# Kernel optimization log

Measured on AMD Instinct MI355X. Metric: run time of the kernel, lower is better.

Reference implementation:

```python
import jax, jax.numpy as jnp
import numpy as np

N_NODES = 150000
N_EDGES = 2400000
N_GRAPHS = 1024
EPS = 1e-5


def setup_inputs() -> dict:
    key = jax.random.key(0)
    ks = jax.random.split(key, 20)
    x = jax.random.normal(ks[0], (N_NODES, 3), dtype=jnp.float32)
    edge_index = jax.random.randint(ks[1], (2, N_EDGES), 0, N_NODES, dtype=jnp.int64)
    batch = jnp.sort(jax.random.randint(ks[2], (N_NODES,), 0, N_GRAPHS, dtype=jnp.int64))

    def glorot(k, shape):
        fan_in, fan_out = shape[0], shape[1]
        lim = jnp.sqrt(6.0 / (fan_in + fan_out)).astype(jnp.float32)
        return jax.random.uniform(k, shape, jnp.float32, -lim, lim)

    params = dict(
        W1=glorot(ks[3], (3, 32)), b1=jnp.zeros((32,), jnp.float32),
        gn1_w=jnp.ones((32,), jnp.float32), gn1_b=jnp.zeros((32,), jnp.float32), gn1_ms=jnp.ones((32,), jnp.float32),
        W2=glorot(ks[4], (32, 32)), b2=jnp.zeros((32,), jnp.float32),
        gn2_w=jnp.ones((32,), jnp.float32), gn2_b=jnp.zeros((32,), jnp.float32), gn2_ms=jnp.ones((32,), jnp.float32),
        W3=glorot(ks[5], (32, 32)), b3=jnp.zeros((32,), jnp.float32),
        gn3_w=jnp.ones((32,), jnp.float32), gn3_b=jnp.zeros((32,), jnp.float32), gn3_ms=jnp.ones((32,), jnp.float32),
        lin_w=glorot(ks[6], (32, 3)), lin_b=jnp.zeros((3,), jnp.float32),
    )
    return dict(x=x, edge_index=edge_index, batch=batch, **params)


def _gcn_conv(x, W, b, src, dst, dinv_sqrt):
    # PyG GCNConv: h = x @ W; propagate with sym-normalized A + self-loops; + bias
    h = x @ W  # [N, F]
    coef = dinv_sqrt[src] * dinv_sqrt[dst]  # [E]
    msgs = h[src] * coef[:, None]  # [E, F]
    agg = jax.ops.segment_sum(msgs, dst, num_segments=N_NODES)
    agg = agg + (dinv_sqrt * dinv_sqrt)[:, None] * h  # self-loop term
    return agg + b


def _graph_norm(x, batch, counts, weight, bias, mean_scale):
    # PyG GraphNorm: per-graph mean/var with learnable mean_scale
    mean = jax.ops.segment_sum(x, batch, num_segments=N_GRAPHS) / counts[:, None]
    out = x - mean_scale * mean[batch]
    var = jax.ops.segment_sum(out * out, batch, num_segments=N_GRAPHS) / counts[:, None]
    std = jnp.sqrt(var + EPS)
    return weight * out / std[batch] + bias


def reference(x, edge_index, batch,
              W1, b1, gn1_w, gn1_b, gn1_ms,
              W2, b2, gn2_w, gn2_b, gn2_ms,
              W3, b3, gn3_w, gn3_b, gn3_ms,
              lin_w, lin_b):
    src, dst = edge_index[0], edge_index[1]
    # degree over A + I (edge weight 1)
    deg = jax.ops.segment_sum(jnp.ones((N_EDGES,), jnp.float32), dst, num_segments=N_NODES) + 1.0
    dinv_sqrt = jax.lax.rsqrt(deg)
    counts = jax.ops.segment_sum(jnp.ones((N_NODES,), jnp.float32), batch, num_segments=N_GRAPHS)

    x1 = jax.nn.relu(_graph_norm(_gcn_conv(x, W1, b1, src, dst, dinv_sqrt), batch, counts, gn1_w, gn1_b, gn1_ms))
    h2 = _graph_norm(_gcn_conv(x1, W2, b2, src, dst, dinv_sqrt), batch, counts, gn2_w, gn2_b, gn2_ms)
    x2 = jax.nn.relu(h2 + x1)
    h3 = _graph_norm(_gcn_conv(x2, W3, b3, src, dst, dinv_sqrt), batch, counts, gn3_w, gn3_b, gn3_ms)
    x3 = jax.nn.relu(h3 + x2)

    pooled = jax.ops.segment_sum(x3, batch, num_segments=N_GRAPHS) / counts[:, None]  # mean pool
    return pooled @ lin_w + lin_b  # [G, 3]
```

## Files before the change

kernel.cpp:

```cpp
#include <hip/hip_runtime.h>

#define N_NODES 150000
#define N_EDGES 2400000
#define N_GRAPHS 1024
#define F 32
#define EPSV 1e-5f

#define BS 256
#define NB ((N_NODES + BS - 1) / BS)
#define CAP 5120
#define EB 8192
#define NEB ((N_EDGES + EB - 1) / EB)
#define EPT (EB / 256)
#define KPT (CAP / 256)

#define SSH 14
#define NS 10

__device__ __forceinline__ float bflo(unsigned int u) {
    union { unsigned int i; float f; } v; v.i = u << 16; return v.f;
}
__device__ __forceinline__ float bfhi(unsigned int u) {
    union { unsigned int i; float f; } v; v.i = u & 0xffff0000u; return v.f;
}
__device__ __forceinline__ unsigned int f2bf(float f) {
    union { float f; unsigned int i; } v; v.f = f;
    unsigned int r = v.i + 0x7fff + ((v.i >> 16) & 1);
    return r >> 16;
}

__global__ void k_init(const int* __restrict__ batch, int* __restrict__ bucketCur,
                       int* __restrict__ off, float* __restrict__ gstats) {
    int i = blockIdx.x * blockDim.x + threadIdx.x;
    if (i >= N_NODES) return;
    if (i < NB) bucketCur[i] = i * CAP;
    if (i < N_GRAPHS * 9) gstats[i] = 0.f;
    int b = batch[i];
    if (i == 0) {
        for (int g = 0; g <= b; ++g) off[g] = 0;
    } else {
        int pb = batch[i - 1];
        for (int g = pb + 1; g <= b; ++g) off[g] = i;
    }
    if (i == N_NODES - 1) {
        for (int g = b + 1; g <= N_GRAPHS; ++g) off[g] = N_NODES;
    }
}

__global__ __launch_bounds__(256) void k_bin(const int* __restrict__ src,
                                             const int* __restrict__ dst,
                                             int* __restrict__ bucketCur,
                                             unsigned int* __restrict__ binned) {
    __shared__ int h[NB];
    __shared__ int gb[NB];
    int t = threadIdx.x;
    for (int b = t; b < NB; b += 256) h[b] = 0;
    __syncthreads();
    int base = blockIdx.x * EB + t;
    unsigned int key[EPT];
    unsigned int pk[EPT];
#pragma unroll
    for (int k = 0; k < EPT; ++k) {
        int e = base + k * 256;
        if (e < N_EDGES) {
            int d = dst[e];
            int b = d >> 8;
            key[k] = ((unsigned int)(d & 255) << 18) | (unsigned int)src[e];
            unsigned int rk = (unsigned int)atomicAdd(&h[b], 1);
            pk[k] = (rk << 10) | (unsigned int)b;
        } else {
            pk[k] = 0xFFFFFFFFu;
        }
    }
    __syncthreads();
    for (int b = t; b < NB; b += 256) {
        int c = h[b];
        gb[b] = c ? atomicAdd(&bucketCur[b], c) : 0;
    }
    __syncthreads();
#pragma unroll
    for (int k = 0; k < EPT; ++k) {
        if (pk[k] != 0xFFFFFFFFu) {
            unsigned int b = pk[k] & 1023u;
            unsigned int rk = pk[k] >> 10;
            binned[gb[b] + rk] = key[k];
        }
    }
}

__global__ __launch_bounds__(256) void k_csr(const unsigned int* __restrict__ binned,
                                             const int* __restrict__ bucketCur,
                                             const float* __restrict__ x,
                                             unsigned int* __restrict__ rowptr,
                                             float* __restrict__ dinv,
                                             float* __restrict__ xs4,
                                             int* __restrict__ csr) {
    __shared__ int cnt[256 * NS];
    __shared__ int pre[256 * NS];
    __shared__ int sc[256];
    int b = blockIdx.x, t = threadIdx.x;
    int e0 = b * CAP;
    int e1 = bucketCur[b];
#pragma unroll
    for (int s = 0; s < NS; ++s) cnt[t * NS + s] = 0;
    __syncthreads();
    unsigned int kc[KPT];
#pragma unroll
    for (int k = 0; k < KPT; ++k) {
        int e = e0 + t + k * 256;
        if (e < e1) {
            kc[k] = binned[e];
            atomicAdd(&cnt[(kc[k] >> 18) * NS + ((kc[k] & 0x3FFFFu) >> SSH)], 1);
        }
    }
    __syncthreads();
    int run = 0;
#pragma unroll
    for (int s = 0; s < NS; ++s) {
        int c = cnt[t * NS + s];
        pre[t * NS + s] = run;
        run += c;
    }
    int v = run;
    sc[t] = v;
    __syncthreads();
    for (int o = 1; o < 256; o <<= 1) {
        int x2 = (t >= o) ? sc[t - o] : 0;
        __syncthreads();
        sc[t] += x2;
        __syncthreads();
    }
    int excl = sc[t] - v;
#pragma unroll
    for (int s = 0; s < NS; ++s) {
        pre[t * NS + s] += excl;
        cnt[t * NS + s] = 0;
    }
    int gnode = b * BS + t;
    if (gnode < N_NODES) {
        rowptr[gnode] = ((unsigned int)(e0 + excl) << 8) | (unsigned int)min(v, 255);
        float dv = rsqrtf((float)v + 1.0f);
        dinv[gnode] = dv;
        float4 xv;
        xv.x = x[gnode * 3 + 0] * dv;
        xv.y = x[gnode * 3 + 1] * dv;
        xv.z = x[gnode * 3 + 2] * dv;
        xv.w = 0.f;
        ((float4*)xs4)[gnode] = xv;
    }
    __syncthreads();
#pragma unroll
    for (int k = 0; k < KPT; ++k) {
        int e = e0 + t + k * 256;
        if (e < e1) {
            unsigned int key = kc[k];
            int idx = (int)(key >> 18) * NS + (int)((key & 0x3FFFFu) >> SSH);
            int pos = atomicAdd(&cnt[idx], 1);
            csr[e0 + pre[idx] + pos] = (int)(key & 0x3FFFFu);
        }
    }
}

__global__ __launch_bounds__(256) void k_gz(
        const float* __restrict__ xs4, const int* __restrict__ csr,
        const unsigned int* __restrict__ rowptr, const float* __restrict__ dinv,
        const int* __restrict__ batch,
        float* __restrict__ zs4, float* __restrict__ gstats) {
    __shared__ float st[8 * 12];
    __shared__ int gbase_s;
    int t = threadIdx.x;
    for (int i = t; i < 8 * 12; i += 256) st[i] = 0.f;
    if (t == 0) gbase_s = batch[blockIdx.x * 128];
    __syncthreads();

    int gid = blockIdx.x * 256 + t;
    int n = gid >> 1, h = gid & 1;
    float z0 = 0.f, z1 = 0.f, z2 = 0.f;
    if (n < N_NODES) {
        const float4* xv = (const float4*)xs4;
        unsigned int rp = rowptr[n];
        int st0 = (int)(rp >> 8);
        int len = (int)(rp & 255u);
        int half0 = (len + 1) >> 1;
        int e  = h ? (st0 + half0) : st0;
        int e1 = h ? (st0 + len)   : (st0 + half0);
        if (!h) {
            float4 sv = xv[n];
            z0 = sv.x; z1 = sv.y; z2 = sv.z;
        }
        for (; e + 3 < e1; e += 4) {
            int s0 = csr[e], s1 = csr[e + 1], s2 = csr[e + 2], s3 = csr[e + 3];
            float4 u0 = xv[s0], u1 = xv[s1], u2 = xv[s2], u3 = xv[s3];
            z0 += u0.x + u1.x + u2.x + u3.x;
            z1 += u0.y + u1.y + u2.y + u3.y;
            z2 += u0.z + u1.z + u2.z + u3.z;
        }
        for (; e < e1; ++e) {
            float4 u = xv[csr[e]];
            z0 += u.x; z1 += u.y; z2 += u.z;
        }
    }
    z0 += __shfl_down(z0, 1);
    z1 += __shfl_down(z1, 1);
    z2 += __shfl_down(z2, 1);
    if (h == 0 && n < N_NODES) {
        float dd = dinv[n];
        z0 *= dd; z1 *= dd; z2 *= dd;
        float4 zv; zv.x = z0; zv.y = z1; zv.z = z2; zv.w = 0.f;
        ((float4*)zs4)[n] = zv;
        int g = batch[n];
        int lg = g - gbase_s;
        if (lg < 8) {
            float* sp = &st[lg * 12];
            atomicAdd(&sp[0], z0);      atomicAdd(&sp[1], z1);
            atomicAdd(&sp[2], z2);      atomicAdd(&sp[3], z0 * z0);
            atomicAdd(&sp[4], z0 * z1); atomicAdd(&sp[5], z0 * z2);
            atomicAdd(&sp[6], z1 * z1); atomicAdd(&sp[7], z1 * z2);
            atomicAdd(&sp[8], z2 * z2);
        } else {
            float* gp = &gstats[g * 9];
            atomicAdd(&gp[0], z0);      atomicAdd(&gp[1], z1);
            atomicAdd(&gp[2], z2);      atomicAdd(&gp[3], z0 * z0);
            atomicAdd(&gp[4], z0 * z1); atomicAdd(&gp[5], z0 * z2);
            atomicAdd(&gp[6], z1 * z1); atomicAdd(&gp[7], z1 * z2);
            atomicAdd(&gp[8], z2 * z2);
        }
    }
    __syncthreads();
    if (t < 72) {
        int slot = t / 9, k = t % 9;
        int g = gbase_s + slot;
        float v = st[slot * 12 + k];
        if (g < N_GRAPHS && v != 0.f) atomicAdd(&gstats[g * 9 + k], v);
    }
}

__global__ __launch_bounds__(256) void k_prep(
        const float* __restrict__ gstats, const int* __restrict__ off,
        const float* __restrict__ W, const float* __restrict__ bias,
        const float* __restrict__ gw, const float* __restrict__ gms,
        float* __restrict__ mvA, float* __restrict__ scA) {
    int gid = blockIdx.x * 256 + threadIdx.x;
    if (gid >= N_GRAPHS * F) return;
    int g = gid >> 5, f = gid & 31;
    float rc = 1.0f / (float)(off[g + 1] - off[g]);
    const float* sp = &gstats[g * 9];
    float S0 = sp[0], S1 = sp[1], S2 = sp[2];
    float m00 = sp[3], m01 = sp[4], m02 = sp[5], m11 = sp[6], m12 = sp[7], m22 = sp[8];
    float w0 = W[0 * F + f], w1 = W[1 * F + f], w2 = W[2 * F + f];
    float b = bias[f];
    float sy = w0 * S0 + w1 * S1 + w2 * S2;
    float m = sy * rc + b;
    float q = w0 * w0 * m00 + w1 * w1 * m11 + w2 * w2 * m22
            + 2.f * (w0 * w1 * m01 + w0 * w2 * m02 + w1 * w2 * m12);
    float Ey2 = q * rc + 2.f * b * (sy * rc) + b * b;
    float mv = gms[f] * m;
    float var = Ey2 - 2.f * mv * m + mv * mv;
    mvA[gid] = mv;
    scA[gid] = gw[f] * rsqrtf(var + EPSV);
}

__global__ __launch_bounds__(256) void k_n1(
        const float* __restrict__ zs4, const int* __restrict__ batch,
        const float* __restrict__ dinv,
        const float* __restrict__ W, const float* __restrict__ bias,
        const float* __restrict__ gb,
        const float* __restrict__ mvA, const float* __restrict__ scA,
        unsigned short* __restrict__ xh, float* __restrict__ outp) {
    int gid = blockIdx.x * 256 + threadIdx.x;
    int n = gid >> 3, c = gid & 7;
    if (n >= N_NODES) return;
    float4 zv = ((const float4*)zs4)[n];
    float z0 = zv.x, z1 = zv.y, z2 = zv.z;
    int g = batch[n];
    float dd = dinv[n];
    float4 w0 = ((const float4*)(W + 0 * F))[c];
    float4 w1 = ((const float4*)(W + 1 * F))[c];
    float4 w2 = ((const float4*)(W + 2 * F))[c];
    float4 y  = ((const float4*)bias)[c];
    y.x += z0 * w0.x + z1 * w1.x + z2 * w2.x;
    y.y += z0 * w0.y + z1 * w1.y + z2 * w2.y;
    y.z += z0 * w0.z + z1 * w1.z + z2 * w2.z;
    y.w += z0 * w0.w + z1 * w1.w + z2 * w2.w;
    float4 mv = ((const float4*)mvA)[g * 8 + c];
    float4 sc = ((const float4*)scA)[g * 8 + c];
    float4 bb = ((const float4*)gb)[c];
    float4 o;
    o.x = fmaxf((y.x - mv.x) * sc.x + bb.x, 0.f);
    o.y = fmaxf((y.y - mv.y) * sc.y + bb.y, 0.f);
    o.z = fmaxf((y.z - mv.z) * sc.z + bb.z, 0.f);
    o.w = fmaxf((y.w - mv.w) * sc.w + bb.w, 0.f);
    ((float4*)outp)[n * 8 + c] = o;
    uint2 hp;
    hp.x = f2bf(o.x * dd) | (f2bf(o.y * dd) << 16);
    hp.y = f2bf(o.z * dd) | (f2bf(o.w * dd) << 16);
    ((uint2*)xh)[n * 8 + c] = hp;
}

#define GAT_CONSUME(U)                                  \
    acc[0] += bflo(U.x); acc[1] += bfhi(U.x);           \
    acc[2] += bflo(U.y); acc[3] += bfhi(U.y);           \
    acc[4] += bflo(U.z); acc[5] += bfhi(U.z);           \
    acc[6] += bflo(U.w); acc[7] += bfhi(U.w);

__global__ __launch_bounds__(256, 8) void k_gat32(
        const unsigned short* __restrict__ xh, const int* __restrict__ csr,
        const unsigned int* __restrict__ rowptr, const float* __restrict__ dinv,
        const float* __restrict__ W, const float* __restrict__ bias,
        float* __restrict__ y) {
    __shared__ float Ws[F * F];
    __shared__ float bs[F];
    __shared__ float Zs[64 * 36];
    int t = threadIdx.x;
    ((float4*)Ws)[t] = ((const float4*)W)[t];
    if (t < F) bs[t] = bias[t];
    __syncthreads();

    int gid = blockIdx.x * 256 + t;
    int n = gid >> 2, c = gid & 3, ln = t >> 2;
    bool act = (n < N_NODES);
    float acc[8];
    if (act) {
        const uint4* xr = (const uint4*)xh;
        uint4 us = xr[n * 4 + c];
        acc[0] = bflo(us.x); acc[1] = bfhi(us.x);
        acc[2] = bflo(us.y); acc[3] = bfhi(us.y);
        acc[4] = bflo(us.z); acc[5] = bfhi(us.z);
        acc[6] = bflo(us.w); acc[7] = bfhi(us.w);
        unsigned int rp = rowptr[n];
        int eb = (int)(rp >> 8);
        int len = (int)(rp & 255u);
        int e1 = eb + len;
        int nch = len >> 2;
        int e = eb;
        if (nch > 0) {
            int a0 = 0, a1 = 0, a2 = 0, a3 = 0;
            uint4 d0, d1, d2, d3;
            {
                int i0 = csr[eb], i1 = csr[eb + 1], i2 = csr[eb + 2], i3 = csr[eb + 3];
                d0 = xr[i0 * 4 + c]; d1 = xr[i1 * 4 + c];
                d2 = xr[i2 * 4 + c]; d3 = xr[i3 * 4 + c];
            }
            if (nch > 1) {
                const int* cp = csr + eb + 4;
                a0 = cp[0]; a1 = cp[1]; a2 = cp[2]; a3 = cp[3];
            }
            for (int ch = 1; ch < nch; ++ch) {
                uint4 t0 = xr[a0 * 4 + c], t1 = xr[a1 * 4 + c];
                uint4 t2 = xr[a2 * 4 + c], t3 = xr[a3 * 4 + c];
                if (ch + 1 < nch) {
                    const int* cp = csr + eb + 4 * (ch + 1);
                    a0 = cp[0]; a1 = cp[1]; a2 = cp[2]; a3 = cp[3];
                }
                GAT_CONSUME(d0) GAT_CONSUME(d1) GAT_CONSUME(d2) GAT_CONSUME(d3)
                d0 = t0; d1 = t1; d2 = t2; d3 = t3;
            }
            GAT_CONSUME(d0) GAT_CONSUME(d1) GAT_CONSUME(d2) GAT_CONSUME(d3)
            e = eb + nch * 4;
        }
        for (; e < e1; ++e) {
            int s0 = csr[e];
            uint4 u0 = xr[s0 * 4 + c];
            GAT_CONSUME(u0)
        }
        float dd = dinv[n];
#pragma unroll
        for (int j = 0; j < 8; ++j) acc[j] *= dd;
    } else {
#pragma unroll
        for (int j = 0; j < 8; ++j) acc[j] = 0.f;
    }
    *(float4*)&Zs[ln * 36 + c * 8]     = *(float4*)&acc[0];
    *(float4*)&Zs[ln * 36 + c * 8 + 4] = *(float4*)&acc[4];
    __syncthreads();

    if (act) {
        const float* zrow = &Zs[ln * 36];
        float4 o0 = ((const float4*)bs)[c * 2];
        float4 o1 = ((const float4*)bs)[c * 2 + 1];
#pragma unroll
        for (int k = 0; k < F; ++k) {
            float zk = zrow[k];
            float4 w0 = ((const float4*)&Ws[k * F])[c * 2];
            float4 w1 = ((const float4*)&Ws[k * F])[c * 2 + 1];
            o0.x += zk * w0.x; o0.y += zk * w0.y; o0.z += zk * w0.z; o0.w += zk * w0.w;
            o1.x += zk * w1.x; o1.y += zk * w1.y; o1.z += zk * w1.z; o1.w += zk * w1.w;
        }
        ((float4*)y)[n * 8 + c * 2]     = o0;
        ((float4*)y)[n * 8 + c * 2 + 1] = o1;
    }
}

template <bool RES, bool WXH>
__global__ __launch_bounds__(256) void k_gn2(
        const float* agg, const float* res, const int* __restrict__ off,
        const float* __restrict__ gw, const float* __restrict__ gb,
        const float* __restrict__ gms, const float* __restrict__ dinv,
        unsigned short* __restrict__ xh, float* outp) {
    __shared__ float red1[256], red2[256];
    __shared__ float mv_s[F], sc_s[F];
    int g = blockIdx.x;
    int i0 = off[g], i1 = off[g + 1];
    float rc = 1.0f / (float)(i1 - i0);
    int t = threadIdx.x;
    int f = t & 31, r0 = t >> 5;

    float s = 0.f, q = 0.f;
    for (int n = i0 + r0; n < i1; n += 8) {
        float v = agg[n * F + f];
        s += v; q += v * v;
    }
    red1[t] = s; red2[t] = q; __syncthreads();
    if (t < 128) { red1[t] += red1[t + 128]; red2[t] += red2[t + 128]; } __syncthreads();
    if (t < 64)  { red1[t] += red1[t + 64];  red2[t] += red2[t + 64];  } __syncthreads();
    if (t < 32) {
        float sm = (red1[t] + red1[t + 32]) * rc;
        float sq = (red2[t] + red2[t + 32]) * rc;
        float mv = gms[t] * sm;
        float var = sq - mv * (2.f * sm - mv);
        mv_s[t] = mv;
        sc_s[t] = gw[t] * rsqrtf(var + EPSV);
    }
    __syncthreads();

    float w = sc_s[f], mv = mv_s[f], bb = gb[f];
    for (int n = i0 + r0; n < i1; n += 8) {
        float y = (agg[n * F + f] - mv) * w + bb;
        if (RES) y += res[n * F + f];
        y = fmaxf(y, 0.f);
        outp[n * F + f] = y;
        if (WXH) xh[n * F + f] = (unsigned short)f2bf(y * dinv[n]);
    }
}

__global__ __launch_bounds__(256) void k_gnfin(
        const float* __restrict__ agg, const float* __restrict__ res,
        const int* __restrict__ off,
        const float* __restrict__ gw, const float* __restrict__ gb,
        const float* __restrict__ gms,
        const float* __restrict__ lin_w, const float* __restrict__ lin_b,
        float* __restrict__ outp) {
    __shared__ float red1[256], red2[256];
    __shared__ float mv_s[F], sc_s[F], pooled_s[F];
    int g = blockIdx.x;
    int i0 = off[g], i1 = off[g + 1];
    float cnt = (float)(i1 - i0);
    float rc = 1.0f / cnt;
    int t = threadIdx.x;
    int f = t & 31, r0 = t >> 5;

    float s = 0.f, q = 0.f;
    for (int n = i0 + r0; n < i1; n += 8) {
        float v = agg[n * F + f];
        s += v; q += v * v;
    }
    red1[t] = s; red2[t] = q; __syncthreads();
    if (t < 128) { red1[t] += red1[t + 128]; red2[t] += red2[t + 128]; } __syncthreads();
    if (t < 64)  { red1[t] += red1[t + 64];  red2[t] += red2[t + 64];  } __syncthreads();
    if (t < 32) {
        float sm = (red1[t] + red1[t + 32]) * rc;
        float sq = (red2[t] + red2[t + 32]) * rc;
        float mv = gms[t] * sm;
        float var = sq - mv * (2.f * sm - mv);
        mv_s[t] = mv;
        sc_s[t] = gw[t] * rsqrtf(var + EPSV);
    }
    __syncthreads();

    float w = sc_s[f], mv = mv_s[f], bb = gb[f];
    float ps = 0.f;
    for (int n = i0 + r0; n < i1; n += 8) {
        float yv = (agg[n * F + f] - mv) * w + bb + res[n * F + f];
        ps += fmaxf(yv, 0.f);
    }
    __syncthreads();
    red1[t] = ps; __syncthreads();
    if (t < 128) red1[t] += red1[t + 128]; __syncthreads();
    if (t < 64)  red1[t] += red1[t + 64];  __syncthreads();
    if (t < 32) { red1[t] += red1[t + 32]; pooled_s[t] = red1[t] * rc; }
    __syncthreads();
    if (t < 3) {
        float o = lin_b[t];
#pragma unroll
        for (int f2 = 0; f2 < F; ++f2) o += pooled_s[f2] * lin_w[f2 * 3 + t];
        outp[g * 3 + t] = o;
    }
}

extern "C" void kernel_launch(void* const* d_in, const int* in_sizes, int n_in,
                              void* d_out, int out_size, void* d_ws, size_t ws_size,
                              hipStream_t stream) {
    const float* x      = (const float*)d_in[0];
    const int*   ei     = (const int*)d_in[1];
    const int*   batch  = (const int*)d_in[2];
    const float* W1     = (const float*)d_in[3];
    const float* b1     = (const float*)d_in[4];
    const float* gn1w   = (const float*)d_in[5];
    const float* gn1b   = (const float*)d_in[6];
    const float* gn1ms  = (const float*)d_in[7];
    const float* W2     = (const float*)d_in[8];
    const float* b2     = (const float*)d_in[9];
    const float* gn2w   = (const float*)d_in[10];
    const float* gn2b   = (const float*)d_in[11];
    const float* gn2ms  = (const float*)d_in[12];
    const float* W3     = (const float*)d_in[13];
    const float* b3     = (const float*)d_in[14];
    const float* gn3w   = (const float*)d_in[15];
    const float* gn3b   = (const float*)d_in[16];
    const float* gn3ms  = (const float*)d_in[17];
    const float* lin_w  = (const float*)d_in[18];
    const float* lin_b  = (const float*)d_in[19];
    float* out = (float*)d_out;

    const int* srcp = ei;
    const int* dstp = ei + N_EDGES;

    char* ws = (char*)d_ws;
    size_t p = 0;
    auto alloc = [&](size_t bytes) {
        size_t r = p; p += (bytes + 511) & ~(size_t)511; return r;
    };
    int*   off       = (int*)  (ws + alloc(sizeof(int) * (N_GRAPHS + 1)));
    int*   bucketCur = (int*)  (ws + alloc(sizeof(int) * NB));
    unsigned int* rowptr = (unsigned int*)(ws + alloc(sizeof(unsigned int) * N_NODES));
    float* dinv      = (float*)(ws + alloc(sizeof(float) * N_NODES));
    float* xs4       = (float*)(ws + alloc(sizeof(float) * N_NODES * 4));
    float* zs4       = (float*)(ws + alloc(sizeof(float) * N_NODES * 4));
    float* gstats    = (float*)(ws + alloc(sizeof(float) * N_GRAPHS * 9));
    float* mvA       = (float*)(ws + alloc(sizeof(float) * N_GRAPHS * F));
    float* scA       = (float*)(ws + alloc(sizeof(float) * N_GRAPHS * F));
    unsigned int* binned = (unsigned int*)(ws + alloc(sizeof(unsigned int) * NB * CAP));
    int*   csr       = (int*)  (ws + alloc(sizeof(int) * NB * CAP));
    float* A         = (float*)(ws + alloc(sizeof(float) * N_NODES * F));
    float* B         = (float*)(ws + alloc(sizeof(float) * N_NODES * F));
    unsigned short* xh = (unsigned short*)binned;
    (void)ws_size; (void)n_in; (void)in_sizes; (void)out_size;

    const int TB = 256;
    dim3 blk(TB);
    int ngrid  = (N_NODES + TB - 1) / TB;
    int ggrid2 = (N_NODES * 2 + TB - 1) / TB;
    int ggrid8 = (N_NODES * 8 + TB - 1) / TB;
    int ggrid4 = (N_NODES * 4 + TB - 1) / TB;

    k_init<<<ngrid, blk, 0, stream>>>(batch, bucketCur, off, gstats);
    k_bin <<<NEB, blk, 0, stream>>>(srcp, dstp, bucketCur, binned);
    k_csr <<<NB, blk, 0, stream>>>(binned, bucketCur, x, rowptr, dinv, xs4, csr);

    k_gz  <<<ggrid2, blk, 0, stream>>>(xs4, csr, rowptr, dinv, batch, zs4, gstats);
    k_prep<<<(N_GRAPHS * F + TB - 1) / TB, blk, 0, stream>>>(
        gstats, off, W1, b1, gn1w, gn1ms, mvA, scA);
    k_n1  <<<ggrid8, blk, 0, stream>>>(zs4, batch, dinv, W1, b1, gn1b, mvA, scA, xh, A);

    k_gat32<<<ggrid4, blk, 0, stream>>>(xh, csr, rowptr, dinv, W2, b2, B);
    k_gn2<true, true><<<N_GRAPHS, blk, 0, stream>>>(
        B, A, off, gn2w, gn2b, gn2ms, dinv, xh, B);

    k_gat32<<<ggrid4, blk, 0, stream>>>(xh, csr, rowptr, dinv, W3, b3, A);
    k_gnfin<<<N_GRAPHS, blk, 0, stream>>>(A, B, off, gn3w, gn3b, gn3ms,
                                          lin_w, lin_b, out);
}
```

Measured before the change: 295.6 us.

## Fuse GraphNorm statistics into aggregation kernel and software-pipeline gather loads in k_gz

The per-graph sum and sum-of-squares for GraphNorm layers 2 and 3 are now accumulated inside k_gat32. Each block first reduces into shared memory for up to four local graphs, falls back to global atomics for other graphs, and then flushes the shared totals with global atomics. k_gn2 and k_gnfin read these precomputed statistics instead of re-reading the full node feature matrix to reduce it, which saves one full pass over the N x 32 activations per layer. The cost is many shared-memory atomics per node, some global atomic contention, and a float-atomic reduction order that is not deterministic. k_gz also gains a software-pipelined prefetch of the next chunk of CSR indices and launch bounds that request higher occupancy.

New measurement: 370.9 us. +25.5%, slower.

```diff
diff --git a/kernel.cpp b/kernel.cpp
--- a/kernel.cpp
+++ b/kernel.cpp
@@ -17,6 +17,8 @@
 #define SSH 14
 #define NS 10
 
+#define GSPAN 4
+
 __device__ __forceinline__ float bflo(unsigned int u) {
     union { unsigned int i; float f; } v; v.i = u << 16; return v.f;
 }
@@ -30,11 +32,13 @@
 }
 
 __global__ void k_init(const int* __restrict__ batch, int* __restrict__ bucketCur,
-                       int* __restrict__ off, float* __restrict__ gstats) {
+                       int* __restrict__ off, float* __restrict__ gstats,
+                       float* __restrict__ gstL) {
     int i = blockIdx.x * blockDim.x + threadIdx.x;
     if (i >= N_NODES) return;
     if (i < NB) bucketCur[i] = i * CAP;
     if (i < N_GRAPHS * 9) gstats[i] = 0.f;
+    if (i < 2 * N_GRAPHS * 2 * F) gstL[i] = 0.f;
     int b = batch[i];
     if (i == 0) {
         for (int g = 0; g <= b; ++g) off[g] = 0;
@@ -161,7 +165,7 @@
     }
 }
 
-__global__ __launch_bounds__(256) void k_gz(
+__global__ __launch_bounds__(256, 8) void k_gz(
         const float* __restrict__ xs4, const int* __restrict__ csr,
         const unsigned int* __restrict__ rowptr, const float* __restrict__ dinv,
         const int* __restrict__ batch,
@@ -188,12 +192,34 @@
             float4 sv = xv[n];
             z0 = sv.x; z1 = sv.y; z2 = sv.z;
         }
-        for (; e + 3 < e1; e += 4) {
-            int s0 = csr[e], s1 = csr[e + 1], s2 = csr[e + 2], s3 = csr[e + 3];
-            float4 u0 = xv[s0], u1 = xv[s1], u2 = xv[s2], u3 = xv[s3];
-            z0 += u0.x + u1.x + u2.x + u3.x;
-            z1 += u0.y + u1.y + u2.y + u3.y;
-            z2 += u0.z + u1.z + u2.z + u3.z;
+        int nch = (e1 - e) >> 2;
+        if (nch > 0) {
+            int eb = e;
+            int a0 = 0, a1 = 0, a2 = 0, a3 = 0;
+            float4 d0, d1, d2, d3;
+            {
+                int i0 = csr[eb], i1 = csr[eb + 1], i2 = csr[eb + 2], i3 = csr[eb + 3];
+                d0 = xv[i0]; d1 = xv[i1]; d2 = xv[i2]; d3 = xv[i3];
+            }
+            if (nch > 1) {
+                const int* cp = csr + eb + 4;
+                a0 = cp[0]; a1 = cp[1]; a2 = cp[2]; a3 = cp[3];
+            }
+            for (int ch = 1; ch < nch; ++ch) {
+                float4 t0 = xv[a0], t1 = xv[a1], t2 = xv[a2], t3 = xv[a3];
+                if (ch + 1 < nch) {
+                    const int* cp = csr + eb + 4 * (ch + 1);
+                    a0 = cp[0]; a1 = cp[1]; a2 = cp[2]; a3 = cp[3];
+                }
+                z0 += d0.x + d1.x + d2.x + d3.x;
+                z1 += d0.y + d1.y + d2.y + d3.y;
+                z2 += d0.z + d1.z + d2.z + d3.z;
+                d0 = t0; d1 = t1; d2 = t2; d3 = t3;
+            }
+            z0 += d0.x + d1.x + d2.x + d3.x;
+            z1 += d0.y + d1.y + d2.y + d3.y;
+            z2 += d0.z + d1.z + d2.z + d3.z;
+            e += nch * 4;
         }
         for (; e < e1; ++e) {
             float4 u = xv[csr[e]];
@@ -306,14 +332,19 @@
 __global__ __launch_bounds__(256, 8) void k_gat32(
         const unsigned short* __restrict__ xh, const int* __restrict__ csr,
         const unsigned int* __restrict__ rowptr, const float* __restrict__ dinv,
+        const int* __restrict__ batch,
         const float* __restrict__ W, const float* __restrict__ bias,
-        float* __restrict__ y) {
+        float* __restrict__ y, float* __restrict__ gst) {
     __shared__ float Ws[F * F];
     __shared__ float bs[F];
     __shared__ float Zs[64 * 36];
+    __shared__ float gst_s[GSPAN * 2 * F];
+    __shared__ int gbase_s;
     int t = threadIdx.x;
     ((float4*)Ws)[t] = ((const float4*)W)[t];
     if (t < F) bs[t] = bias[t];
+    gst_s[t] = 0.f;
+    if (t == 0) gbase_s = batch[blockIdx.x * 64];
     __syncthreads();
 
     int gid = blockIdx.x * 256 + t;
@@ -388,6 +419,32 @@
         }
         ((float4*)y)[n * 8 + c * 2]     = o0;
         ((float4*)y)[n * 8 + c * 2 + 1] = o1;
+
+        int g = batch[n];
+        int lg = g - gbase_s;
+        float vv[8] = {o0.x, o0.y, o0.z, o0.w, o1.x, o1.y, o1.z, o1.w};
+        if (lg < GSPAN) {
+            float* sp = &gst_s[lg * 2 * F];
+#pragma unroll
+            for (int j = 0; j < 8; ++j) {
+                atomicAdd(&sp[c * 8 + j], vv[j]);
+                atomicAdd(&sp[F + c * 8 + j], vv[j] * vv[j]);
+            }
+        } else {
+            float* gp = &gst[g * 2 * F];
+#pragma unroll
+            for (int j = 0; j < 8; ++j) {
+                atomicAdd(&gp[c * 8 + j], vv[j]);
+                atomicAdd(&gp[F + c * 8 + j], vv[j] * vv[j]);
+            }
+        }
+    }
+    __syncthreads();
+    {
+        int lg = t >> 6, idx = t & 63;
+        int g = gbase_s + lg;
+        float v = gst_s[lg * 2 * F + idx];
+        if (g < N_GRAPHS && v != 0.f) atomicAdd(&gst[g * 2 * F + idx], v);
     }
 }
 
@@ -396,8 +453,8 @@
         const float* agg, const float* res, const int* __restrict__ off,
         const float* __restrict__ gw, const float* __restrict__ gb,
         const float* __restrict__ gms, const float* __restrict__ dinv,
+        const float* __restrict__ gst,
         unsigned short* __restrict__ xh, float* outp) {
-    __shared__ float red1[256], red2[256];
     __shared__ float mv_s[F], sc_s[F];
     int g = blockIdx.x;
     int i0 = off[g], i1 = off[g + 1];
@@ -405,17 +462,9 @@
     int t = threadIdx.x;
     int f = t & 31, r0 = t >> 5;
 
-    float s = 0.f, q = 0.f;
-    for (int n = i0 + r0; n < i1; n += 8) {
-        float v = agg[n * F + f];
-        s += v; q += v * v;
-    }
-    red1[t] = s; red2[t] = q; __syncthreads();
-    if (t < 128) { red1[t] += red1[t + 128]; red2[t] += red2[t + 128]; } __syncthreads();
-    if (t < 64)  { red1[t] += red1[t + 64];  red2[t] += red2[t + 64];  } __syncthreads();
-    if (t < 32) {
-        float sm = (red1[t] + red1[t + 32]) * rc;
-        float sq = (red2[t] + red2[t + 32]) * rc;
+    if (t < F) {
+        float sm = gst[g * 2 * F + t] * rc;
+        float sq = gst[g * 2 * F + F + t] * rc;
         float mv = gms[t] * sm;
         float var = sq - mv * (2.f * sm - mv);
         mv_s[t] = mv;
@@ -437,29 +486,20 @@
         const float* __restrict__ agg, const float* __restrict__ res,
         const int* __restrict__ off,
         const float* __restrict__ gw, const float* __restrict__ gb,
-        const float* __restrict__ gms,
+        const float* __restrict__ gms, const float* __restrict__ gst,
         const float* __restrict__ lin_w, const float* __restrict__ lin_b,
         float* __restrict__ outp) {
-    __shared__ float red1[256], red2[256];
+    __shared__ float red1[256];
     __shared__ float mv_s[F], sc_s[F], pooled_s[F];
     int g = blockIdx.x;
     int i0 = off[g], i1 = off[g + 1];
-    float cnt = (float)(i1 - i0);
-    float rc = 1.0f / cnt;
+    float rc = 1.0f / (float)(i1 - i0);
     int t = threadIdx.x;
     int f = t & 31, r0 = t >> 5;
 
-    float s = 0.f, q = 0.f;
-    for (int n = i0 + r0; n < i1; n += 8) {
-        float v = agg[n * F + f];
-        s += v; q += v * v;
-    }
-    red1[t] = s; red2[t] = q; __syncthreads();
-    if (t < 128) { red1[t] += red1[t + 128]; red2[t] += red2[t + 128]; } __syncthreads();
-    if (t < 64)  { red1[t] += red1[t + 64];  red2[t] += red2[t + 64];  } __syncthreads();
-    if (t < 32) {
-        float sm = (red1[t] + red1[t + 32]) * rc;
-        float sq = (red2[t] + red2[t + 32]) * rc;
+    if (t < F) {
+        float sm = gst[g * 2 * F + t] * rc;
+        float sq = gst[g * 2 * F + F + t] * rc;
         float mv = gms[t] * sm;
         float var = sq - mv * (2.f * sm - mv);
         mv_s[t] = mv;
@@ -473,7 +513,6 @@
         float yv = (agg[n * F + f] - mv) * w + bb + res[n * F + f];
         ps += fmaxf(yv, 0.f);
     }
-    __syncthreads();
     red1[t] = ps; __syncthreads();
     if (t < 128) red1[t] += red1[t + 128]; __syncthreads();
     if (t < 64)  red1[t] += red1[t + 64];  __syncthreads();
@@ -529,11 +568,14 @@
     float* gstats    = (float*)(ws + alloc(sizeof(float) * N_GRAPHS * 9));
     float* mvA       = (float*)(ws + alloc(sizeof(float) * N_GRAPHS * F));
     float* scA       = (float*)(ws + alloc(sizeof(float) * N_GRAPHS * F));
+    float* gstL      = (float*)(ws + alloc(sizeof(float) * 2 * N_GRAPHS * 2 * F));
     unsigned int* binned = (unsigned int*)(ws + alloc(sizeof(unsigned int) * NB * CAP));
     int*   csr       = (int*)  (ws + alloc(sizeof(int) * NB * CAP));
     float* A         = (float*)(ws + alloc(sizeof(float) * N_NODES * F));
     float* B         = (float*)(ws + alloc(sizeof(float) * N_NODES * F));
     unsigned short* xh = (unsigned short*)binned;
+    float* gstL2 = gstL;
+    float* gstL3 = gstL + N_GRAPHS * 2 * F;
     (void)ws_size; (void)n_in; (void)in_sizes; (void)out_size;
 
     const int TB = 256;
@@ -543,7 +585,7 @@
     int ggrid8 = (N_NODES * 8 + TB - 1) / TB;
     int ggrid4 = (N_NODES * 4 + TB - 1) / TB;
 
-    k_init<<<ngrid, blk, 0, stream>>>(batch, bucketCur, off, gstats);
+    k_init<<<ngrid, blk, 0, stream>>>(batch, bucketCur, off, gstats, gstL);
     k_bin <<<NEB, blk, 0, stream>>>(srcp, dstp, bucketCur, binned);
     k_csr <<<NB, blk, 0, stream>>>(binned, bucketCur, x, rowptr, dinv, xs4, csr);
 
@@ -552,11 +594,11 @@
         gstats, off, W1, b1, gn1w, gn1ms, mvA, scA);
     k_n1  <<<ggrid8, blk, 0, stream>>>(zs4, batch, dinv, W1, b1, gn1b, mvA, scA, xh, A);
 
-    k_gat32<<<ggrid4, blk, 0, stream>>>(xh, csr, rowptr, dinv, W2, b2, B);
+    k_gat32<<<ggrid4, blk, 0, stream>>>(xh, csr, rowptr, dinv, batch, W2, b2, B, gstL2);
     k_gn2<true, true><<<N_GRAPHS, blk, 0, stream>>>(
-        B, A, off, gn2w, gn2b, gn2ms, dinv, xh, B);
-
-    k_gat32<<<ggrid4, blk, 0, stream>>>(xh, csr, rowptr, dinv, W3, b3, A);
-    k_gnfin<<<N_GRAPHS, blk, 0, stream>>>(A, B, off, gn3w, gn3b, gn3ms,
+        B, A, off, gn2w, gn2b, gn2ms, dinv, gstL2, xh, B);
+
+    k_gat32<<<ggrid4, blk, 0, stream>>>(xh, csr, rowptr, dinv, batch, W3, b3, A, gstL3);
+    k_gnfin<<<N_GRAPHS, blk, 0, stream>>>(A, B, off, gn3w, gn3b, gn3ms, gstL3,
                                           lin_w, lin_b, out);
 }
```
